# Kernel optimization log

Measured on AMD Instinct MI355X. Metric: run time of the kernel, lower is better.

The kernel has to match this reference:

```python
import jax, jax.numpy as jnp
import numpy as np

B, N, DIM = 2, 2048, 2048
N_HEAD, N_KV_HEAD = 32, 8
HEAD_DIM = DIM // N_HEAD  # 64
NEG_INF = -1e9


def setup_inputs() -> dict:
    key = jax.random.key(0)
    ks = jax.random.split(key, 4)
    x = jax.random.normal(ks[0], (B, N, DIM), dtype=jnp.float32)
    Wq = jax.random.normal(ks[1], (DIM, N_HEAD * HEAD_DIM), dtype=jnp.float32) * (DIM ** -0.5)
    Wkv = jax.random.normal(ks[2], (DIM, 2 * N_KV_HEAD * HEAD_DIM), dtype=jnp.float32) * (DIM ** -0.5)
    Wo = jax.random.normal(ks[3], (N_HEAD * HEAD_DIM, DIM), dtype=jnp.float32) * (DIM ** -0.5)
    # RoPE angles: freqs = 1/theta^(2i/d), angle[p, i] = p * freqs[i]
    freqs = 1.0 / (10000.0 ** (jnp.arange(0, HEAD_DIM, 2, dtype=jnp.float32) / HEAD_DIM))
    angles = jnp.arange(N, dtype=jnp.float32)[:, None] * freqs[None, :]  # (N, HEAD_DIM//2)
    rope_cos = jnp.cos(angles)
    rope_sin = jnp.sin(angles)
    # additive causal mask (n, n)
    mask = jnp.where(jnp.tril(jnp.ones((N, N), dtype=bool)), 0.0, NEG_INF).astype(jnp.float32)
    return {"x": x, "Wq": Wq, "Wkv": Wkv, "Wo": Wo, "rope_cos": rope_cos, "rope_sin": rope_sin, "mask": mask, "start_pos": 0}


def apply_rope(x, cos, sin):
    # x: (b, n, h, d); cos/sin: (n, d//2). Complex mult on interleaved pairs.
    xr = x.reshape(*x.shape[:-1], HEAD_DIM // 2, 2)
    xe, xo = xr[..., 0], xr[..., 1]
    c = cos[None, :, None, :]
    s = sin[None, :, None, :]
    yr = xe * c - xo * s
    yi = xe * s + xo * c
    return jnp.stack([yr, yi], axis=-1).reshape(x.shape)


def reference(x, Wq, Wkv, Wo, rope_cos, rope_sin, mask, start_pos):
    b, n, _ = x.shape
    q = (x @ Wq).reshape(b, n, N_HEAD, HEAD_DIM)
    kv = (x @ Wkv).reshape(b, n, 2, N_KV_HEAD, HEAD_DIM)
    k, v = kv[:, :, 0], kv[:, :, 1]
    q = apply_rope(q, rope_cos, rope_sin)
    k = apply_rope(k, rope_cos, rope_sin)
    # repeat kv heads: 'b n h d -> b n (r h) d'
    r = N_HEAD // N_KV_HEAD
    k = jnp.tile(k, (1, 1, r, 1))
    v = jnp.tile(v, (1, 1, r, 1))
    scale = HEAD_DIM ** -0.5
    attn = jnp.einsum('bnhd,bmhd->bhnm', q, k) * scale + mask[None, None]
    attn = jax.nn.softmax(attn, axis=-1)
    out = jnp.einsum('bhnm,bmhd->bnhd', attn, v).reshape(b, n, N_HEAD * HEAD_DIM)
    return out @ Wo
```

## Files before the change

### kernel.cpp

```cpp
#include <hip/hip_runtime.h>


#define BSZ  2
#define NSEQ 2048
#define DIMD 2048
#define NH   32
#define NKV  8
#define HD   64

typedef __bf16 bf16x8 __attribute__((ext_vector_type(8)));
typedef __bf16 bf16x4 __attribute__((ext_vector_type(4)));
typedef __bf16 bf16x2 __attribute__((ext_vector_type(2)));
typedef float  floatx4 __attribute__((ext_vector_type(4)));

#define MFMA16(a, b, c) __builtin_amdgcn_mfma_f32_16x16x32_bf16(a, b, c, 0, 0, 0)

__device__ __forceinline__ void gload_lds16(const void* g, void* l) {
    __builtin_amdgcn_global_load_lds((const __attribute__((address_space(1))) void*)g,
                                     (__attribute__((address_space(3))) void*)l, 16, 0, 0);
}

__global__ void cvt_x_kernel(const float* __restrict__ in, __bf16* __restrict__ out, int n4) {
    int i = blockIdx.x * blockDim.x + threadIdx.x;
    if (i >= n4) return;
    float4 v = ((const float4*)in)[i];
    bf16x4 o;
    o[0] = (__bf16)v.x; o[1] = (__bf16)v.y; o[2] = (__bf16)v.z; o[3] = (__bf16)v.w;
    ((bf16x4*)out)[i] = o;
}

__global__ void transpose_cvt_kernel(const float* __restrict__ W, __bf16* __restrict__ Wt,
                                     int C, int K) {
    __shared__ float t[32][33];
    int c0 = blockIdx.x * 32, r0 = blockIdx.y * 32;
    int lx = threadIdx.x & 31, ly = threadIdx.x >> 5;
    for (int i = 0; i < 32; i += 8)
        t[ly + i][lx] = W[(size_t)(r0 + ly + i) * C + c0 + lx];
    __syncthreads();
    for (int i = 0; i < 32; i += 8)
        Wt[(size_t)(c0 + ly + i) * K + r0 + lx] = (__bf16)t[lx][ly + i];
}

__global__ __launch_bounds__(256) void gemm_qkv_kernel(
    const __bf16* __restrict__ A, const __bf16* __restrict__ Bt,
    const float* __restrict__ cosb, const float* __restrict__ sinb,
    __bf16* __restrict__ Qo, __bf16* __restrict__ Ko, __bf16* __restrict__ Vo) {
    __shared__ __align__(16) __bf16 As[128 * 64];
    __shared__ __align__(16) __bf16 Bs[128 * 64];
    __shared__ bf16x2 trig[128 * 33];

    int tid = threadIdx.x;
    int wave = tid >> 6, lane = tid & 63;
    int wr = wave >> 1, wc = wave & 1;
    int quad = lane >> 4, l16 = lane & 15;
    int t0 = blockIdx.y * 128;
    int p0 = blockIdx.x * 128;
    bool isV = (p0 >= 2560);

    if (!isV) {
        const float* cb = cosb + (size_t)(t0 & 2047) * 32;
        const float* sb = sinb + (size_t)(t0 & 2047) * 32;
        for (int i4 = tid; i4 < 1024; i4 += 256) {
            int idx = i4 * 4, row = idx >> 5, col = idx & 31;
            float4 cv = *(const float4*)(cb + idx);
            float4 sv4 = *(const float4*)(sb + idx);
            bf16x2* d = &trig[row * 33 + col];
            bf16x2 e0, e1, e2, e3;
            e0[0] = (__bf16)cv.x; e0[1] = (__bf16)sv4.x;
            e1[0] = (__bf16)cv.y; e1[1] = (__bf16)sv4.y;
            e2[0] = (__bf16)cv.z; e2[1] = (__bf16)sv4.z;
            e3[0] = (__bf16)cv.w; e3[1] = (__bf16)sv4.w;
            d[0] = e0; d[1] = e1; d[2] = e2; d[3] = e3;
        }
    }

    floatx4 acc[4][4] = {};
    const __bf16* Abase = A + (size_t)t0 * DIMD;
    const __bf16* Bbase = Bt + (size_t)p0 * DIMD;
    int sw8 = (l16 & 7) << 3;

    for (int k0 = 0; k0 < DIMD; k0 += 64) {
        __syncthreads();
        for (int r = 0; r < 4; ++r) {
            int obase = r * 2048 + wave * 512;
            int o = obase + lane * 8;
            int row = o >> 6;
            int el = (o & 63) ^ ((row & 7) << 3);
            gload_lds16(Abase + (size_t)row * DIMD + k0 + el, &As[obase]);
            gload_lds16(Bbase + (size_t)row * DIMD + k0 + el, &Bs[obase]);
        }
        __syncthreads();
        for (int c = 0; c < 2; ++c) {
            int ko = (c * 32 + quad * 8) ^ sw8;
            bf16x8 tf[4], pf[4];
            for (int j = 0; j < 4; ++j)
                tf[j] = *(const bf16x8*)&As[(wr * 64 + j * 16 + l16) * 64 + ko];
            for (int i = 0; i < 4; ++i)
                pf[i] = *(const bf16x8*)&Bs[(wc * 64 + i * 16 + l16) * 64 + ko];
            for (int i = 0; i < 4; ++i)
                for (int j = 0; j < 4; ++j)
                    acc[i][j] = MFMA16(pf[i], tf[j], acc[i][j]);
        }
    }

    for (int j = 0; j < 4; ++j) {
        int nl = wr * 64 + j * 16 + l16;
        int t = t0 + nl;
        int b = t >> 11, n = t & 2047;
        for (int i = 0; i < 4; ++i) {
            float x0 = acc[i][j][0], x1 = acc[i][j][1];
            float x2 = acc[i][j][2], x3 = acc[i][j][3];
            int dq = i * 16 + quad * 4;
            if (!isV) {
                int d2 = dq >> 1;
                bf16x2 cs0 = trig[nl * 33 + d2];
                bf16x2 cs1 = trig[nl * 33 + d2 + 1];
                float c0 = (float)cs0[0], s0 = (float)cs0[1];
                float c1 = (float)cs1[0], s1 = (float)cs1[1];
                bf16x4 o;
                o[0] = (__bf16)(x0 * c0 - x1 * s0);
                o[1] = (__bf16)(x0 * s0 + x1 * c0);
                o[2] = (__bf16)(x2 * c1 - x3 * s1);
                o[3] = (__bf16)(x2 * s1 + x3 * c1);
                if (p0 < 2048) {
                    int h = (p0 >> 6) + wc;
                    *(bf16x4*)&Qo[((size_t)(b * NH + h) * NSEQ + n) * HD + dq] = o;
                } else {
                    int kvh = ((p0 - 2048) >> 6) + wc;
                    *(bf16x4*)&Ko[((size_t)(b * NKV + kvh) * NSEQ + n) * HD + dq] = o;
                }
            } else {
                int kvh = ((p0 - 2560) >> 6) + wc;
                size_t base = ((size_t)(b * NKV + kvh)) * HD;
                Vo[(base + dq + 0) * NSEQ + n] = (__bf16)x0;
                Vo[(base + dq + 1) * NSEQ + n] = (__bf16)x1;
                Vo[(base + dq + 2) * NSEQ + n] = (__bf16)x2;
                Vo[(base + dq + 3) * NSEQ + n] = (__bf16)x3;
            }
        }
    }
}

__global__ __launch_bounds__(256) void gemm_bt_kernel(
    const __bf16* __restrict__ A, const __bf16* __restrict__ Bt,
    float* __restrict__ C, int M, int N, int K) {
    __shared__ __align__(16) __bf16 As[128 * 64];
    __shared__ __align__(16) __bf16 Bs[128 * 64];
    int tid = threadIdx.x;
    int wave = tid >> 6, lane = tid & 63;
    int wr = wave >> 1, wc = wave & 1;
    int quad = lane >> 4, l16 = lane & 15;
    int m0 = blockIdx.y * 128, n0 = blockIdx.x * 128;

    floatx4 acc[4][4] = {};
    const __bf16* Abase = A + (size_t)m0 * K;
    const __bf16* Bbase = Bt + (size_t)n0 * K;
    int sw8 = (l16 & 7) << 3;

    for (int k0 = 0; k0 < K; k0 += 64) {
        __syncthreads();
        for (int r = 0; r < 4; ++r) {
            int obase = r * 2048 + wave * 512;
            int o = obase + lane * 8;
            int row = o >> 6;
            int el = (o & 63) ^ ((row & 7) << 3);
            gload_lds16(Abase + (size_t)row * K + k0 + el, &As[obase]);
            gload_lds16(Bbase + (size_t)row * K + k0 + el, &Bs[obase]);
        }
        __syncthreads();
        for (int c = 0; c < 2; ++c) {
            int ko = (c * 32 + quad * 8) ^ sw8;
            bf16x8 af[4], bfr[4];
            for (int i = 0; i < 4; ++i)
                af[i] = *(const bf16x8*)&As[(wr * 64 + i * 16 + l16) * 64 + ko];
            for (int j = 0; j < 4; ++j)
                bfr[j] = *(const bf16x8*)&Bs[(wc * 64 + j * 16 + l16) * 64 + ko];
            for (int i = 0; i < 4; ++i)
                for (int j = 0; j < 4; ++j)
                    acc[i][j] = MFMA16(af[i], bfr[j], acc[i][j]);
        }
    }
    for (int i = 0; i < 4; ++i) {
        int row = m0 + wr * 64 + i * 16 + quad * 4;
        for (int j = 0; j < 4; ++j) {
            int col = n0 + wc * 64 + j * 16 + l16;
            float* Cp = C + (size_t)row * N + col;
            for (int r = 0; r < 4; ++r)
                Cp[(size_t)r * N] = acc[i][j][r];
        }
    }
}

__global__ __launch_bounds__(256) void attn_kernel(
    const __bf16* __restrict__ Q, const __bf16* __restrict__ K,
    const __bf16* __restrict__ Vt, __bf16* __restrict__ O) {
    __shared__ __align__(16) __bf16 Kl[128 * 64];
    __shared__ __align__(16) __bf16 Vl[64 * 128];
    __shared__ __align__(16) __bf16 Pl[4][16 * 136];

    int tid = threadIdx.x;
    int wave = tid >> 6, lane = tid & 63;
    int quad = lane >> 4, l16 = lane & 15;
    int bk = blockIdx.x;
    int b = bk >> 3, kvh = bk & 7;
    int h = kvh + wave * 8;

    const __bf16* Qbase = Q + ((size_t)(b * NH + h)) * NSEQ * HD;
    const __bf16* Kbase = K + ((size_t)(b * NKV + kvh)) * NSEQ * HD;
    const __bf16* Vbase = Vt + ((size_t)(b * NKV + kvh)) * HD * NSEQ;
    __bf16* P = &Pl[wave][0];
    const float c2 = 0.125f * 1.44269504f;
    int swk = (l16 & 7) << 3;
    int swv = l16 << 3;

    for (int half = 0; half < 2; ++half) {
        int qt = half ? blockIdx.y : 63 - blockIdx.y;
        int q0 = qt * 32;

        bf16x8 qf[2][2];
        for (int s = 0; s < 2; ++s) {
            int qrow = q0 + s * 16 + l16;
            qf[s][0] = *(const bf16x8*)(Qbase + (size_t)qrow * HD + quad * 8);
            qf[s][1] = *(const bf16x8*)(Qbase + (size_t)qrow * HD + 32 + quad * 8);
        }

        floatx4 oa[2][4] = {};
        float l_[2] = {0.0f, 0.0f};
        int ktmax = (q0 + 31) >> 7;

        for (int kt = 0; kt <= ktmax; ++kt) {
            __syncthreads();
            for (int r = 0; r < 4; ++r) {
                int obase = r * 2048 + wave * 512;
                int o = obase + lane * 8;
                int krow = o >> 6;
                int kel = (o & 63) ^ ((krow & 7) << 3);
                gload_lds16(Kbase + (size_t)kt * 8192 + krow * 64 + kel, &Kl[obase]);
                int vrow = o >> 7;
                int vel = (o & 127) ^ ((vrow & 15) << 3);
                gload_lds16(Vbase + (size_t)vrow * NSEQ + kt * 128 + vel, &Vl[obase]);
            }
            __syncthreads();

            bool diag = (kt == ktmax);
            int rel0 = q0 - kt * 128;
            for (int s = 0; s < 2; ++s) {
                int cmax = diag ? ((rel0 + s * 16 + 15) >> 5) : 3;
                if (cmax > 3) cmax = 3;
                int jmax = diag ? (2 * cmax + 1) : 7;
                int q_l = q0 + s * 16 + l16;

                for (int j = 0; j <= jmax; ++j) {
                    int krr = (j * 16 + l16) * 64;
                    bf16x8 k0 = *(const bf16x8*)&Kl[krr + ((quad * 8) ^ swk)];
                    bf16x8 k1 = *(const bf16x8*)&Kl[krr + ((quad * 8 + 32) ^ swk)];
                    floatx4 sv = {0.f, 0.f, 0.f, 0.f};
                    sv = MFMA16(k0, qf[s][0], sv);
                    sv = MFMA16(k1, qf[s][1], sv);
                    int kvb = kt * 128 + j * 16 + quad * 4;
                    bf16x4 pk;
                    if (diag) {
                        for (int r = 0; r < 4; ++r) {
                            float p = __builtin_exp2f(sv[r] * c2);
                            if (kvb + r > q_l) p = 0.0f;
                            l_[s] += p;
                            pk[r] = (__bf16)p;
                        }
                    } else {
                        for (int r = 0; r < 4; ++r) {
                            float p = __builtin_exp2f(sv[r] * c2);
                            l_[s] += p;
                            pk[r] = (__bf16)p;
                        }
                    }
                    *(bf16x4*)&P[l16 * 136 + j * 16 + quad * 4] = pk;
                }

                for (int c = 0; c <= cmax; ++c) {
                    bf16x8 pb = *(const bf16x8*)&P[l16 * 136 + c * 32 + quad * 8];
                    int vo = (c * 32 + quad * 8);
                    for (int jd = 0; jd < 4; ++jd) {
                        bf16x8 vf = *(const bf16x8*)&Vl[(jd * 16 + l16) * 128 + (vo ^ swv)];
                        oa[s][jd] = MFMA16(vf, pb, oa[s][jd]);
                    }
                }
            }
        }

        for (int s = 0; s < 2; ++s) {
            float lf = l_[s];
            lf += __shfl_xor(lf, 16, 64);
            lf += __shfl_xor(lf, 32, 64);
            float inv = 1.0f / lf;
            int n = q0 + s * 16 + l16;
            __bf16* Op = O + ((size_t)(b * NSEQ + n)) * (NH * HD) + h * HD + quad * 4;
            for (int jd = 0; jd < 4; ++jd) {
                bf16x4 ov;
                for (int r = 0; r < 4; ++r) ov[r] = (__bf16)(oa[s][jd][r] * inv);
                *(bf16x4*)(Op + jd * 16) = ov;
            }
        }
    }
}

extern "C" void kernel_launch(void* const* d_in, const int* in_sizes, int n_in,
                              void* d_out, int out_size, void* d_ws, size_t ws_size,
                              hipStream_t stream) {
    const float* x   = (const float*)d_in[0];
    const float* Wq  = (const float*)d_in[1];
    const float* Wkv = (const float*)d_in[2];
    const float* Wo  = (const float*)d_in[3];
    const float* rc  = (const float*)d_in[4];
    const float* rs  = (const float*)d_in[5];
    float* out = (float*)d_out;
    char* ws = (char*)d_ws;

    __bf16* xb    = (__bf16*)(ws + 0);
    __bf16* wqkvt = (__bf16*)(ws + 16777216);
    __bf16* wot   = (__bf16*)(ws + 29360128);
    __bf16* Qb    = (__bf16*)(ws + 37748736);
    __bf16* Kb    = (__bf16*)(ws + 54525952);
    __bf16* Vtb   = (__bf16*)(ws + 58720256);
    __bf16* attnb = (__bf16*)(ws + 62914560);

    cvt_x_kernel<<<8192, 256, 0, stream>>>(x, xb, 2097152);
    transpose_cvt_kernel<<<dim3(64, 64), 256, 0, stream>>>(Wq, wqkvt, 2048, 2048);
    transpose_cvt_kernel<<<dim3(32, 64), 256, 0, stream>>>(Wkv, wqkvt + (size_t)2048 * 2048, 1024, 2048);
    transpose_cvt_kernel<<<dim3(64, 64), 256, 0, stream>>>(Wo, wot, 2048, 2048);

    gemm_qkv_kernel<<<dim3(24, 32), 256, 0, stream>>>(xb, wqkvt, rc, rs, Qb, Kb, Vtb);

    attn_kernel<<<dim3(16, 32), 256, 0, stream>>>(Qb, Kb, Vtb, attnb);

    gemm_bt_kernel<<<dim3(16, 32), 256, 0, stream>>>(attnb, wot, out, 4096, 2048, 2048);
}
```

Baseline: 354.7 us.

## Double-buffer LDS tiles in output GEMM and attention with smaller KV tiles

The output-projection GEMM now keeps two LDS buffers and issues the async global-to-LDS loads for the next K slice before computing on the current one, so each iteration needs one barrier instead of two. The attention kernel drops its KV tile from 128 to 64 keys and double-buffers it the same way, including prefetching the first tile of the second query half. It also loads all K and V fragments into registers once per tile and drops the diagonal-tile column limit, so some masked work on the diagonal tile is still computed. The goal is to hide global load latency behind MFMA work and cut barrier stalls, at the cost of more registers and more, smaller loop iterations.

```diff
diff --git a/kernel.cpp b/kernel.cpp
--- a/kernel.cpp
+++ b/kernel.cpp
@@ -141,11 +141,11 @@
     }
 }
 
-__global__ __launch_bounds__(256) void gemm_bt_kernel(
+__global__ __launch_bounds__(256) void gemm_bt_db_kernel(
     const __bf16* __restrict__ A, const __bf16* __restrict__ Bt,
     float* __restrict__ C, int M, int N, int K) {
-    __shared__ __align__(16) __bf16 As[128 * 64];
-    __shared__ __align__(16) __bf16 Bs[128 * 64];
+    __shared__ __align__(16) __bf16 As[2][128 * 64];
+    __shared__ __align__(16) __bf16 Bs[2][128 * 64];
     int tid = threadIdx.x;
     int wave = tid >> 6, lane = tid & 63;
     int wr = wave >> 1, wc = wave & 1;
@@ -157,28 +157,34 @@
     const __bf16* Bbase = Bt + (size_t)n0 * K;
     int sw8 = (l16 & 7) << 3;
 
-    for (int k0 = 0; k0 < K; k0 += 64) {
-        __syncthreads();
+    auto stage = [&](int k0, int bi) {
         for (int r = 0; r < 4; ++r) {
             int obase = r * 2048 + wave * 512;
             int o = obase + lane * 8;
             int row = o >> 6;
             int el = (o & 63) ^ ((row & 7) << 3);
-            gload_lds16(Abase + (size_t)row * K + k0 + el, &As[obase]);
-            gload_lds16(Bbase + (size_t)row * K + k0 + el, &Bs[obase]);
-        }
+            gload_lds16(Abase + (size_t)row * K + k0 + el, &As[bi][obase]);
+            gload_lds16(Bbase + (size_t)row * K + k0 + el, &Bs[bi][obase]);
+        }
+    };
+
+    stage(0, 0);
+    int pb = 0;
+    for (int k0 = 0; k0 < K; k0 += 64) {
         __syncthreads();
+        if (k0 + 64 < K) stage(k0 + 64, pb ^ 1);
         for (int c = 0; c < 2; ++c) {
             int ko = (c * 32 + quad * 8) ^ sw8;
             bf16x8 af[4], bfr[4];
             for (int i = 0; i < 4; ++i)
-                af[i] = *(const bf16x8*)&As[(wr * 64 + i * 16 + l16) * 64 + ko];
+                af[i] = *(const bf16x8*)&As[pb][(wr * 64 + i * 16 + l16) * 64 + ko];
             for (int j = 0; j < 4; ++j)
-                bfr[j] = *(const bf16x8*)&Bs[(wc * 64 + j * 16 + l16) * 64 + ko];
+                bfr[j] = *(const bf16x8*)&Bs[pb][(wc * 64 + j * 16 + l16) * 64 + ko];
             for (int i = 0; i < 4; ++i)
                 for (int j = 0; j < 4; ++j)
                     acc[i][j] = MFMA16(af[i], bfr[j], acc[i][j]);
         }
+        pb ^= 1;
     }
     for (int i = 0; i < 4; ++i) {
         int row = m0 + wr * 64 + i * 16 + quad * 4;
@@ -194,9 +200,9 @@
 __global__ __launch_bounds__(256) void attn_kernel(
     const __bf16* __restrict__ Q, const __bf16* __restrict__ K,
     const __bf16* __restrict__ Vt, __bf16* __restrict__ O) {
-    __shared__ __align__(16) __bf16 Kl[128 * 64];
-    __shared__ __align__(16) __bf16 Vl[64 * 128];
-    __shared__ __align__(16) __bf16 Pl[4][16 * 136];
+    __shared__ __align__(16) __bf16 Kl[2][64 * 64];
+    __shared__ __align__(16) __bf16 Vl[2][64 * 64];
+    __shared__ __align__(16) __bf16 Pl[4][16 * 72];
 
     int tid = threadIdx.x;
     int wave = tid >> 6, lane = tid & 63;
@@ -211,7 +217,20 @@
     __bf16* P = &Pl[wave][0];
     const float c2 = 0.125f * 1.44269504f;
     int swk = (l16 & 7) << 3;
-    int swv = l16 << 3;
+
+    auto stage = [&](int kt, int bi) {
+        for (int r = 0; r < 2; ++r) {
+            int obase = r * 2048 + wave * 512;
+            int o = obase + lane * 8;
+            int row = o >> 6;
+            int el = (o & 63) ^ ((row & 7) << 3);
+            gload_lds16(Kbase + (size_t)kt * 4096 + row * 64 + el, &Kl[bi][obase]);
+            gload_lds16(Vbase + (size_t)row * NSEQ + kt * 64 + el, &Vl[bi][obase]);
+        }
+    };
+
+    int pb = 0;
+    stage(0, 0);
 
     for (int half = 0; half < 2; ++half) {
         int qt = half ? blockIdx.y : 63 - blockIdx.y;
@@ -226,40 +245,32 @@
 
         floatx4 oa[2][4] = {};
         float l_[2] = {0.0f, 0.0f};
-        int ktmax = (q0 + 31) >> 7;
+        int ktmax = (q0 + 31) >> 6;
 
         for (int kt = 0; kt <= ktmax; ++kt) {
             __syncthreads();
-            for (int r = 0; r < 4; ++r) {
-                int obase = r * 2048 + wave * 512;
-                int o = obase + lane * 8;
-                int krow = o >> 6;
-                int kel = (o & 63) ^ ((krow & 7) << 3);
-                gload_lds16(Kbase + (size_t)kt * 8192 + krow * 64 + kel, &Kl[obase]);
-                int vrow = o >> 7;
-                int vel = (o & 127) ^ ((vrow & 15) << 3);
-                gload_lds16(Vbase + (size_t)vrow * NSEQ + kt * 128 + vel, &Vl[obase]);
+            if (kt < ktmax) stage(kt + 1, pb ^ 1);
+            else if (half == 0) stage(0, pb ^ 1);
+
+            bf16x8 kf[4][2], vf[4][2];
+            for (int j = 0; j < 4; ++j) {
+                int rr = (j * 16 + l16) * 64;
+                kf[j][0] = *(const bf16x8*)&Kl[pb][rr + ((quad * 8) ^ swk)];
+                kf[j][1] = *(const bf16x8*)&Kl[pb][rr + ((quad * 8 + 32) ^ swk)];
+                vf[j][0] = *(const bf16x8*)&Vl[pb][rr + ((quad * 8) ^ swk)];
+                vf[j][1] = *(const bf16x8*)&Vl[pb][rr + ((quad * 8 + 32) ^ swk)];
             }
-            __syncthreads();
 
             bool diag = (kt == ktmax);
-            int rel0 = q0 - kt * 128;
             for (int s = 0; s < 2; ++s) {
-                int cmax = diag ? ((rel0 + s * 16 + 15) >> 5) : 3;
-                if (cmax > 3) cmax = 3;
-                int jmax = diag ? (2 * cmax + 1) : 7;
                 int q_l = q0 + s * 16 + l16;
-
-                for (int j = 0; j <= jmax; ++j) {
-                    int krr = (j * 16 + l16) * 64;
-                    bf16x8 k0 = *(const bf16x8*)&Kl[krr + ((quad * 8) ^ swk)];
-                    bf16x8 k1 = *(const bf16x8*)&Kl[krr + ((quad * 8 + 32) ^ swk)];
+                for (int j = 0; j < 4; ++j) {
                     floatx4 sv = {0.f, 0.f, 0.f, 0.f};
-                    sv = MFMA16(k0, qf[s][0], sv);
-                    sv = MFMA16(k1, qf[s][1], sv);
-                    int kvb = kt * 128 + j * 16 + quad * 4;
+                    sv = MFMA16(kf[j][0], qf[s][0], sv);
+                    sv = MFMA16(kf[j][1], qf[s][1], sv);
                     bf16x4 pk;
                     if (diag) {
+                        int kvb = kt * 64 + j * 16 + quad * 4;
                         for (int r = 0; r < 4; ++r) {
                             float p = __builtin_exp2f(sv[r] * c2);
                             if (kvb + r > q_l) p = 0.0f;
@@ -273,18 +284,16 @@
                             pk[r] = (__bf16)p;
                         }
                     }
-                    *(bf16x4*)&P[l16 * 136 + j * 16 + quad * 4] = pk;
+                    *(bf16x4*)&P[l16 * 72 + j * 16 + quad * 4] = pk;
                 }
-
-                for (int c = 0; c <= cmax; ++c) {
-                    bf16x8 pb = *(const bf16x8*)&P[l16 * 136 + c * 32 + quad * 8];
-                    int vo = (c * 32 + quad * 8);
-                    for (int jd = 0; jd < 4; ++jd) {
-                        bf16x8 vf = *(const bf16x8*)&Vl[(jd * 16 + l16) * 128 + (vo ^ swv)];
-                        oa[s][jd] = MFMA16(vf, pb, oa[s][jd]);
-                    }
+                bf16x8 pb0 = *(const bf16x8*)&P[l16 * 72 + quad * 8];
+                bf16x8 pb1 = *(const bf16x8*)&P[l16 * 72 + 32 + quad * 8];
+                for (int j = 0; j < 4; ++j) {
+                    oa[s][j] = MFMA16(vf[j][0], pb0, oa[s][j]);
+                    oa[s][j] = MFMA16(vf[j][1], pb1, oa[s][j]);
                 }
             }
+            pb ^= 1;
         }
 
         for (int s = 0; s < 2; ++s) {
@@ -294,10 +303,10 @@
             float inv = 1.0f / lf;
             int n = q0 + s * 16 + l16;
             __bf16* Op = O + ((size_t)(b * NSEQ + n)) * (NH * HD) + h * HD + quad * 4;
-            for (int jd = 0; jd < 4; ++jd) {
+            for (int j = 0; j < 4; ++j) {
                 bf16x4 ov;
-                for (int r = 0; r < 4; ++r) ov[r] = (__bf16)(oa[s][jd][r] * inv);
-                *(bf16x4*)(Op + jd * 16) = ov;
+                for (int r = 0; r < 4; ++r) ov[r] = (__bf16)(oa[s][j][r] * inv);
+                *(bf16x4*)(Op + j * 16) = ov;
             }
         }
     }
@@ -332,5 +341,5 @@
 
     attn_kernel<<<dim3(16, 32), 256, 0, stream>>>(Qb, Kb, Vtb, attnb);
 
-    gemm_bt_kernel<<<dim3(16, 32), 256, 0, stream>>>(attnb, wot, out, 4096, 2048, 2048);
-}
+    gemm_bt_db_kernel<<<dim3(16, 32), 256, 0, stream>>>(attnb, wot, out, 4096, 2048, 2048);
+}
```

Measured after the change: 328.4 us. 7.4% less time.
